# Optimization experiments

Hardware: AMD Instinct MI355X
Metric: run time of the kernel (lower is better)

Reference implementation:

```python
import jax, jax.numpy as jnp
import numpy as np

H, DQS, DQP, DVS, DVP = 12, 16, 4, 16, 8
S_SCALAR = (3.0 * DQS) ** -0.5
S_POINT = (3.0 * DQP * (9.0 * 2.0 ** 0.5)) ** -0.5
S_PAIR = 3.0 ** -0.5
_OFF = np.cumsum([0, H * DQS, H * DQS, H * DVS, H * DQP * 3, H * DQP * 3, H * DVP * 3])


def _ln(x, g, b, eps=1e-5):
    mu = x.mean(-1, keepdims=True)
    var = x.var(-1, keepdims=True)
    return (x - mu) / jnp.sqrt(var + eps) * g + b


def setup_inputs() -> dict:
    B, N, D, PD = 2, 512, 384, 128
    key = jax.random.key(0)
    ks = jax.random.split(key, 12)
    node_feats = jax.random.normal(ks[0], (B, N, D), jnp.float32)
    pair_feats = jax.random.normal(ks[1], (B, N, N, PD), jnp.float32)
    mask = jnp.ones((B, N), dtype=bool)
    # random per-residue rigid frames (orthonormal rotations via QR)
    rot = jnp.linalg.qr(jax.random.normal(ks[2], (B, N, 3, 3), jnp.float32))[0]
    trans = jax.random.normal(ks[3], (B, N, 3), jnp.float32)
    dim_qkv = int(_OFF[-1])             # 1152
    dim_out = H * (PD + DVS + 4 * DVP)  # 2112
    s = 0.02
    p = dict(
        ln_s_g=jnp.ones((D,)), ln_s_b=jnp.zeros((D,)),
        ln_p_g=jnp.ones((PD,)), ln_p_b=jnp.zeros((PD,)),
        w_pair_bias=s * jax.random.normal(ks[4], (PD, H), jnp.float32),
        w_qkv=s * jax.random.normal(ks[5], (D, dim_qkv), jnp.float32),
        point_weights=jnp.full((1, H, 1, 1), float(np.log(np.e - 1.0)), jnp.float32),
        w_out=s * jax.random.normal(ks[6], (dim_out, D), jnp.float32),
        b_out=jnp.zeros((D,)),
        ln_t_g=jnp.ones((D,)), ln_t_b=jnp.zeros((D,)),
        w_ff1=s * jax.random.normal(ks[7], (D, 4 * D), jnp.float32),
        b_ff1=jnp.zeros((4 * D,)),
        w_ff2=s * jax.random.normal(ks[8], (4 * D, D), jnp.float32),
        b_ff2=jnp.zeros((D,)),
    )
    return dict(node_feats=node_feats, pair_feats=pair_feats, mask=mask,
                rot=rot, trans=trans, **p)


def reference(node_feats, pair_feats, mask, rot, trans,
              ln_s_g, ln_s_b, ln_p_g, ln_p_b, w_pair_bias, w_qkv,
              point_weights, w_out, b_out,
              ln_t_g, ln_t_b, w_ff1, b_ff1, w_ff2, b_ff2):
    b, n, d = node_feats.shape
    x = _ln(node_feats, ln_s_g, ln_s_b)
    p = _ln(pair_feats, ln_p_g, ln_p_b)
    pair_bias = jnp.einsum('bijd,dh->bhij', p, w_pair_bias)
    qkv = x @ w_qkv  # (b,n,1152)

    def heads(t, dh):
        return t.reshape(b, n, H, dh).transpose(0, 2, 1, 3)  # b h n d

    q_s = heads(qkv[..., _OFF[0]:_OFF[1]], DQS)
    k_s = heads(qkv[..., _OFF[1]:_OFF[2]], DQS)
    v_s = heads(qkv[..., _OFF[2]:_OFF[3]], DVS)

    def to_pts(t, dp):
        pts = t.reshape(b, n, H * dp, 3)
        # rigid apply: R_i @ x + t_i (global frame)
        pts = jnp.einsum('bnxy,bnpy->bnpx', rot, pts) + trans[:, :, None, :]
        return pts.reshape(b, n, H, dp, 3).transpose(0, 2, 1, 3, 4)  # b h n d 3

    q_p = to_pts(qkv[..., _OFF[3]:_OFF[4]], DQP)
    k_p = to_pts(qkv[..., _OFF[4]:_OFF[5]], DQP)
    v_p = to_pts(qkv[..., _OFF[5]:_OFF[6]], DVP)

    scalar_logits = jnp.einsum('bhid,bhjd->bhij', q_s, k_s)
    # dist attn: -sum_{d,c} (q-k)^2, expanded to avoid (b,h,n,n,d,3) intermediate
    qq = jnp.sum(q_p * q_p, axis=(-1, -2))
    kk = jnp.sum(k_p * k_p, axis=(-1, -2))
    qk = jnp.einsum('bhidc,bhjdc->bhij', q_p, k_p)
    point_logits = -(qq[..., :, None] + kk[..., None, :] - 2.0 * qk)
    point_logits = point_logits * jax.nn.softplus(point_weights)

    neg = jnp.finfo(node_feats.dtype).min
    pm = mask[:, None, :, None] & mask[:, None, None, :]  # b 1 i j
    scalar_logits = jnp.where(pm, scalar_logits, neg)
    point_logits = jnp.where(pm, point_logits, neg)
    pair_bias = jnp.where(pm, pair_bias, neg)

    logits = S_SCALAR * scalar_logits + S_POINT * point_logits + S_PAIR * pair_bias
    attn = jax.nn.softmax(logits, axis=-1)

    out_s = jnp.einsum('bhij,bhjd->bhid', attn, v_s)
    out_pair = jnp.einsum('bhij,bijd->bhid', attn, p)
    out_p = jnp.einsum('bhij,bhjdc->bhidc', attn, v_p)
    # rigid inverse: R_i^T (x - t_i) back to local frame
    pts = out_p.transpose(0, 2, 1, 3, 4).reshape(b, n, H * DVP, 3)
    pts = jnp.einsum('bnyx,bnpy->bnpx', rot, pts - trans[:, :, None, :])
    out_p = pts.reshape(b, n, H, DVP, 3)
    pnorm = jnp.sqrt(jnp.sum(out_p * out_p, axis=-1) + 1e-8)  # safe_norm

    cat = jnp.concatenate([
        out_s.transpose(0, 2, 1, 3).reshape(b, n, H * DVS),
        out_p.reshape(b, n, H * DVP * 3),
        pnorm.reshape(b, n, H * DVP),
        out_pair.transpose(0, 2, 1, 3).reshape(b, n, -1),
    ], axis=-1)
    attn_out = cat @ w_out + b_out

    # residuals + transition (dropout=0 -> identity). Note: transition is
    # applied to attn_out (pre-residual), exactly as in the torch forward.
    node1 = attn_out + node_feats
    t = _ln(attn_out, ln_t_g, ln_t_b)
    t = jax.nn.gelu(t @ w_ff1 + b_ff1) @ w_ff2 + b_ff2
    return t + node1
```

## Files before the change

### kernel.cpp

```cpp
#include <hip/hip_runtime.h>
#include <hip/hip_bf16.h>
#include <math.h>

typedef __hip_bfloat16 bf16;
typedef _Float16 f16;
typedef unsigned short ushort_t;
typedef ushort_t ushort8 __attribute__((ext_vector_type(8)));
typedef ushort_t us4 __attribute__((ext_vector_type(4)));
typedef short bf16x8 __attribute__((ext_vector_type(8)));
typedef f16 f16x8 __attribute__((ext_vector_type(8)));
typedef f16 f16x2 __attribute__((ext_vector_type(2)));
typedef float f32x4 __attribute__((ext_vector_type(4)));
typedef unsigned int u32x4 __attribute__((ext_vector_type(4)));

constexpr float S_SCALAR = 0.14433756729740643f;
constexpr float S_POINT  = 0.08091531528f;
constexpr float S_PAIR   = 0.5773502691896258f;

__device__ inline short f2bfs(float x) {
  return (short)__builtin_bit_cast(unsigned short, __float2bfloat16(x));
}
__device__ inline ushort_t f2bfu(float x) {
  return (ushort_t)__builtin_bit_cast(unsigned short, __float2bfloat16(x));
}
__device__ inline ushort_t f2hu(float x) {
  return __builtin_bit_cast(ushort_t, (f16)x);
}
__device__ inline float h2f(ushort_t u) {
  return (float)__builtin_bit_cast(f16, u);
}
__device__ inline float fdot2f(unsigned a, unsigned b, float c) {
#if __has_builtin(__builtin_amdgcn_fdot2)
  return __builtin_amdgcn_fdot2(__builtin_bit_cast(f16x2, a),
                                __builtin_bit_cast(f16x2, b), c, false);
#else
  f16x2 av = __builtin_bit_cast(f16x2, a), bv = __builtin_bit_cast(f16x2, b);
  return c + (float)av[0] * (float)bv[0] + (float)av[1] * (float)bv[1];
#endif
}

__device__ inline float gelu_tanh(float x) {
  float c = 0.7978845608028654f * (x + 0.044715f * x * x * x);
  return 0.5f * x * (1.f + tanhf(c));
}

__global__ __launch_bounds__(128) void ln384_kernel(
    const float* __restrict__ in, const float* __restrict__ g,
    const float* __restrict__ b, float* __restrict__ out)
{
  int row = blockIdx.x;
  const float* x = in + (size_t)row * 384;
  int t = threadIdx.x;
  float v[3]; float s = 0.f, s2 = 0.f;
#pragma unroll
  for (int i = 0; i < 3; i++) { v[i] = x[t + 128 * i]; s += v[i]; s2 += v[i] * v[i]; }
  for (int o = 32; o; o >>= 1) { s += __shfl_down(s, o); s2 += __shfl_down(s2, o); }
  __shared__ float sh[4];
  int wid = t >> 6, lane = t & 63;
  if (lane == 0) { sh[wid] = s; sh[2 + wid] = s2; }
  __syncthreads();
  s = sh[0] + sh[1]; s2 = sh[2] + sh[3];
  float mean = s * (1.f / 384.f);
  float var = s2 * (1.f / 384.f) - mean * mean;
  float rstd = rsqrtf(fmaxf(var, 0.f) + 1e-5f);
  float* orow = out + (size_t)row * 384;
#pragma unroll
  for (int i = 0; i < 3; i++) {
    int c = t + 128 * i;
    orow[c] = (v[i] - mean) * rstd * g[c] + b[c];
  }
}

__global__ __launch_bounds__(256) void prep_all_kernel(
    const float* __restrict__ w_qkv, const float* __restrict__ w_out,
    const float* __restrict__ w_ff1, const float* __restrict__ w_ff2,
    ushort_t* __restrict__ wqkvT, ushort_t* __restrict__ woutT,
    ushort_t* __restrict__ wff1T, ushort_t* __restrict__ wff2T,
    const float* __restrict__ g, const float* __restrict__ bb,
    const float* __restrict__ wpb, ushort_t* __restrict__ gwbT,
    float* __restrict__ gsbs,
    const float* __restrict__ node, const float* __restrict__ ln_s_g,
    const float* __restrict__ ln_s_b, float* __restrict__ xout)
{
  __shared__ float shmem[2048];
  int bid = blockIdx.x;
  int t = threadIdx.x;
  if (bid < 2376) {
    const float* src; ushort_t* dst; int K, N, bx, by;
    if (bid < 432)       { src = w_qkv; dst = wqkvT; K = 384;  N = 1152; bx = bid % 36;          by = bid / 36; }
    else if (bid < 1224) { src = w_out; dst = woutT; K = 2112; N = 384;  bx = (bid - 432) % 12;  by = (bid - 432) / 12; }
    else if (bid < 1800) { src = w_ff1; dst = wff1T; K = 384;  N = 1536; bx = (bid - 1224) % 48; by = (bid - 1224) / 48; }
    else                 { src = w_ff2; dst = wff2T; K = 1536; N = 384;  bx = (bid - 1800) % 12; by = (bid - 1800) / 12; }
    float (&tile)[32][33] = *reinterpret_cast<float (*)[32][33]>(shmem);
    int n0 = bx * 32, k0 = by * 32;
    int c = t & 31, r4 = (t >> 5) * 4;
#pragma unroll
    for (int i = 0; i < 4; i++)
      tile[r4 + i][c] = src[(size_t)(k0 + r4 + i) * N + n0 + c];
    __syncthreads();
#pragma unroll
    for (int i = 0; i < 4; i++)
      dst[(size_t)(n0 + r4 + i) * K + k0 + c] = f2bfu(tile[c][r4 + i]);
    return;
  }
  if (bid == 2376) {
    for (int idx = t; idx < 2048; idx += 256) {
      int h = idx >> 7, c = idx & 127;
      float v = (h < 12) ? g[c] * wpb[c * 12 + h] : 0.f;
      bf16 r = __float2bfloat16(v);
      gwbT[idx] = __builtin_bit_cast(unsigned short, r);
      shmem[idx] = __bfloat162float(r);
    }
    __syncthreads();
    if (t < 16) {
      float s = 0.f;
      for (int c = 0; c < 128; c++) s += shmem[t * 128 + c];
      gsbs[t] = s;
    } else if (t < 32) {
      int h = t - 16;
      float s = 0.f;
      if (h < 12) for (int c = 0; c < 128; c++) s = fmaf(bb[c], wpb[c * 12 + h], s);
      gsbs[t] = s;
    }
    return;
  }
  int half = t >> 7, tt = t & 127;
  int row = (bid - 2377) * 2 + half;
  const float* x = node + (size_t)row * 384;
  float v[3]; float s = 0.f, s2 = 0.f;
#pragma unroll
  for (int i = 0; i < 3; i++) { v[i] = x[tt + 128 * i]; s += v[i]; s2 += v[i] * v[i]; }
  for (int o = 32; o; o >>= 1) { s += __shfl_down(s, o); s2 += __shfl_down(s2, o); }
  int wid = t >> 6, lane = t & 63;
  if (lane == 0) { shmem[wid] = s; shmem[4 + wid] = s2; }
  __syncthreads();
  s = shmem[half * 2] + shmem[half * 2 + 1];
  s2 = shmem[4 + half * 2] + shmem[4 + half * 2 + 1];
  float mean = s * (1.f / 384.f);
  float var = s2 * (1.f / 384.f) - mean * mean;
  float rstd = rsqrtf(fmaxf(var, 0.f) + 1e-5f);
  float* orow = xout + (size_t)row * 384;
#pragma unroll
  for (int i = 0; i < 3; i++) {
    int c = tt + 128 * i;
    orow[c] = (v[i] - mean) * rstd * ln_s_g[c] + ln_s_b[c];
  }
}

template <int EPI>
__global__ __launch_bounds__(256) void gemm_mfma_kernel(
    const float* __restrict__ A, const ushort_t* __restrict__ BT,
    const float* __restrict__ bias, const float* __restrict__ r1,
    const float* __restrict__ r2, float* __restrict__ C,
    int M, int Nn, int K)
{
  __shared__ ushort_t As[64][72];
  __shared__ ushort_t Bs[64][72];
  int t = threadIdx.x;
  int w = t >> 6, l = t & 63;
  int m0 = blockIdx.y * 64, n0 = blockIdx.x * 64;
  int wm = (w >> 1) * 32, wn = (w & 1) * 32;
  int lr = l & 15, lk = l >> 4;
  int sr = t >> 2, sc = (t & 3) * 16;
  f32x4 acc[2][2];
#pragma unroll
  for (int i = 0; i < 2; i++)
#pragma unroll
    for (int j = 0; j < 2; j++) acc[i][j] = (f32x4){0.f, 0.f, 0.f, 0.f};

  for (int k0 = 0; k0 < K; k0 += 64) {
    const float* Ar = A + (size_t)(m0 + sr) * K + k0 + sc;
    const ushort_t* Br = BT + (size_t)(n0 + sr) * K + k0 + sc;
    float4 a0 = *(const float4*)(Ar + 0);
    float4 a1 = *(const float4*)(Ar + 4);
    float4 a2 = *(const float4*)(Ar + 8);
    float4 a3 = *(const float4*)(Ar + 12);
    ushort8 b0 = *(const ushort8*)(Br + 0);
    ushort8 b1 = *(const ushort8*)(Br + 8);
    ushort8 u0, u1;
    u0[0] = f2bfu(a0.x); u0[1] = f2bfu(a0.y); u0[2] = f2bfu(a0.z); u0[3] = f2bfu(a0.w);
    u0[4] = f2bfu(a1.x); u0[5] = f2bfu(a1.y); u0[6] = f2bfu(a1.z); u0[7] = f2bfu(a1.w);
    u1[0] = f2bfu(a2.x); u1[1] = f2bfu(a2.y); u1[2] = f2bfu(a2.z); u1[3] = f2bfu(a2.w);
    u1[4] = f2bfu(a3.x); u1[5] = f2bfu(a3.y); u1[6] = f2bfu(a3.z); u1[7] = f2bfu(a3.w);
    *(ushort8*)&As[sr][sc] = u0;
    *(ushort8*)&As[sr][sc + 8] = u1;
    *(ushort8*)&Bs[sr][sc] = b0;
    *(ushort8*)&Bs[sr][sc + 8] = b1;
    __syncthreads();
#pragma unroll
    for (int kk = 0; kk < 2; kk++) {
      bf16x8 af0 = *(const bf16x8*)&As[wm + lr][kk * 32 + lk * 8];
      bf16x8 af1 = *(const bf16x8*)&As[wm + 16 + lr][kk * 32 + lk * 8];
      bf16x8 bf0 = *(const bf16x8*)&Bs[wn + lr][kk * 32 + lk * 8];
      bf16x8 bf1 = *(const bf16x8*)&Bs[wn + 16 + lr][kk * 32 + lk * 8];
      acc[0][0] = __builtin_amdgcn_mfma_f32_16x16x32_bf16(af0, bf0, acc[0][0], 0, 0, 0);
      acc[0][1] = __builtin_amdgcn_mfma_f32_16x16x32_bf16(af0, bf1, acc[0][1], 0, 0, 0);
      acc[1][0] = __builtin_amdgcn_mfma_f32_16x16x32_bf16(af1, bf0, acc[1][0], 0, 0, 0);
      acc[1][1] = __builtin_amdgcn_mfma_f32_16x16x32_bf16(af1, bf1, acc[1][1], 0, 0, 0);
    }
    __syncthreads();
  }
#pragma unroll
  for (int mf = 0; mf < 2; mf++) {
#pragma unroll
    for (int nf = 0; nf < 2; nf++) {
      int nn = n0 + wn + nf * 16 + lr;
      float bv = bias ? bias[nn] : 0.f;
#pragma unroll
      for (int e = 0; e < 4; e++) {
        int m = m0 + wm + mf * 16 + lk * 4 + e;
        float v = acc[mf][nf][e] + bv;
        if (EPI == 1) v = gelu_tanh(v);
        if (EPI == 2) v += r1[(size_t)m * Nn + nn] + r2[(size_t)m * Nn + nn];
        C[(size_t)m * Nn + nn] = v;
      }
    }
  }
}

template <int EPI>
__global__ __launch_bounds__(256) void gemm_mfma_m32_kernel(
    const float* __restrict__ A, const ushort_t* __restrict__ BT,
    const float* __restrict__ bias, const float* __restrict__ r1,
    const float* __restrict__ r2, float* __restrict__ C,
    int M, int Nn, int K)
{
  __shared__ ushort_t As[32][72];
  __shared__ ushort_t Bs[64][72];
  int t = threadIdx.x;
  int w = t >> 6, l = t & 63;
  int m0 = blockIdx.y * 32, n0 = blockIdx.x * 64;
  int wm = (w & 1) * 16, wn = (w >> 1) * 32;
  int lr = l & 15, lk = l >> 4;
  int ar = t >> 3, ac = (t & 7) * 8;
  int br = t >> 2, bc = (t & 3) * 16;
  f32x4 acc[2];
  acc[0] = (f32x4){0.f, 0.f, 0.f, 0.f};
  acc[1] = (f32x4){0.f, 0.f, 0.f, 0.f};

  for (int k0 = 0; k0 < K; k0 += 64) {
    const float* Ar = A + (size_t)(m0 + ar) * K + k0 + ac;
    float4 a0 = *(const float4*)(Ar + 0);
    float4 a1 = *(const float4*)(Ar + 4);
    ushort8 u;
    u[0] = f2bfu(a0.x); u[1] = f2bfu(a0.y); u[2] = f2bfu(a0.z); u[3] = f2bfu(a0.w);
    u[4] = f2bfu(a1.x); u[5] = f2bfu(a1.y); u[6] = f2bfu(a1.z); u[7] = f2bfu(a1.w);
    *(ushort8*)&As[ar][ac] = u;
    const ushort_t* Br = BT + (size_t)(n0 + br) * K + k0 + bc;
    *(ushort8*)&Bs[br][bc] = *(const ushort8*)(Br + 0);
    *(ushort8*)&Bs[br][bc + 8] = *(const ushort8*)(Br + 8);
    __syncthreads();
#pragma unroll
    for (int kk = 0; kk < 2; kk++) {
      bf16x8 af = *(const bf16x8*)&As[wm + lr][kk * 32 + lk * 8];
      bf16x8 bf0 = *(const bf16x8*)&Bs[wn + lr][kk * 32 + lk * 8];
      bf16x8 bf1 = *(const bf16x8*)&Bs[wn + 16 + lr][kk * 32 + lk * 8];
      acc[0] = __builtin_amdgcn_mfma_f32_16x16x32_bf16(af, bf0, acc[0], 0, 0, 0);
      acc[1] = __builtin_amdgcn_mfma_f32_16x16x32_bf16(af, bf1, acc[1], 0, 0, 0);
    }
    __syncthreads();
  }
#pragma unroll
  for (int nf = 0; nf < 2; nf++) {
    int nn = n0 + wn + nf * 16 + lr;
    float bv = bias ? bias[nn] : 0.f;
#pragma unroll
    for (int e = 0; e < 4; e++) {
      int m = m0 + wm + lk * 4 + e;
      float v = acc[nf][e] + bv;
      if (EPI == 1) v = gelu_tanh(v);
      if (EPI == 2) v += r1[(size_t)m * Nn + nn] + r2[(size_t)m * Nn + nn];
      C[(size_t)m * Nn + nn] = v;
    }
  }
}

__global__ __launch_bounds__(256) void qkv_post_kernel(
    const float* __restrict__ qkv, const float* __restrict__ rot,
    const float* __restrict__ trans, const float* __restrict__ pw,
    f16* __restrict__ qhat, ushort_t* __restrict__ khatP,
    ushort_t* __restrict__ vT)
{
  int bh = blockIdx.x;
  int b = bh / 12, h = bh - b * 12;
  int role = blockIdx.y >> 1;
  int j = (blockIdx.y & 1) * 256 + threadIdx.x;
  int bn = b * 512 + j;
  const float* row = qkv + (size_t)bn * 1152;
  float R[9];
#pragma unroll
  for (int k = 0; k < 9; k++) R[k] = rot[bn * 9 + k];
  float T0 = trans[bn * 3], T1 = trans[bn * 3 + 1], T2 = trans[bn * 3 + 2];
  if (role == 0) {
    float sp = log1pf(__expf(pw[h]));
    float c1 = 2.f * S_POINT * sp;
    float spp = S_POINT * sp;
    f16* qh = qhat + ((size_t)bh * 512 + j) * 32;
#pragma unroll
    for (int d = 0; d < 16; d++) qh[d] = (f16)(S_SCALAR * row[h * 16 + d]);
#pragma unroll
    for (int p = 0; p < 4; p++) {
      int base = 576 + (h * 4 + p) * 3;
      float x = row[base], y = row[base + 1], z = row[base + 2];
      qh[16 + p * 3 + 0] = (f16)(c1 * (R[0] * x + R[1] * y + R[2] * z + T0));
      qh[16 + p * 3 + 1] = (f16)(c1 * (R[3] * x + R[4] * y + R[5] * z + T1));
      qh[16 + p * 3 + 2] = (f16)(c1 * (R[6] * x + R[7] * y + R[8] * z + T2));
    }
    qh[28] = (f16)(-spp);
    qh[29] = (f16)0.f; qh[30] = (f16)0.f; qh[31] = (f16)0.f;
  } else if (role == 1) {
    float kv[32];
#pragma unroll
    for (int d = 0; d < 16; d++) kv[d] = row[192 + h * 16 + d];
    float kksum = 0.f;
#pragma unroll
    for (int p = 0; p < 4; p++) {
      int base = 720 + (h * 4 + p) * 3;
      float x = row[base], y = row[base + 1], z = row[base + 2];
      float gx = R[0] * x + R[1] * y + R[2] * z + T0;
      float gy = R[3] * x + R[4] * y + R[5] * z + T1;
      float gz = R[6] * x + R[7] * y + R[8] * z + T2;
      kv[16 + p * 3 + 0] = gx; kv[16 + p * 3 + 1] = gy; kv[16 + p * 3 + 2] = gz;
      kksum = fmaf(gx, gx, kksum); kksum = fmaf(gy, gy, kksum); kksum = fmaf(gz, gz, kksum);
    }
    kv[28] = kksum; kv[29] = 0.f; kv[30] = 0.f; kv[31] = 0.f;
    ushort_t* kp = khatP + ((size_t)bh * 4) * 512 * 8 + (size_t)j * 8;
#pragma unroll
    for (int dg = 0; dg < 4; dg++) {
      ushort8 u;
#pragma unroll
      for (int e = 0; e < 8; e++) u[e] = f2hu(kv[dg * 8 + e]);
      *(ushort8*)(kp + (size_t)dg * 512 * 8) = u;
    }
  } else {
    ushort_t* vt = vT + (size_t)bh * 40 * 512;
#pragma unroll
    for (int c = 0; c < 16; c++) vt[c * 512 + j] = f2hu(row[384 + h * 16 + c]);
#pragma unroll
    for (int p = 0; p < 8; p++) {
      int base = 864 + (h * 8 + p) * 3;
      float x = row[base], y = row[base + 1], z = row[base + 2];
      vt[(16 + p * 3 + 0) * 512 + j] = f2hu(R[0] * x + R[1] * y + R[2] * z + T0);
      vt[(16 + p * 3 + 1) * 512 + j] = f2hu(R[3] * x + R[4] * y + R[5] * z + T1);
      vt[(16 + p * 3 + 2) * 512 + j] = f2hu(R[6] * x + R[7] * y + R[8] * z + T2);
    }
  }
}

__global__ __launch_bounds__(256, 2) void mega_kernel(
    const float* __restrict__ pair, const ushort_t* __restrict__ gwbT,
    const float* __restrict__ gsbs, const float* __restrict__ g,
    const float* __restrict__ bb, const f16* __restrict__ qhat,
    const ushort_t* __restrict__ khatP, ushort_t* __restrict__ attnb,
    float* __restrict__ cat)
{
  __shared__ ushort_t tile[128][136];
  __shared__ ushort_t Ps[12][520];
  __shared__ ushort_t bias_s[12][136];
  __shared__ unsigned qhat_u[12][16];
  __shared__ float m_s[12], l_s[12], r_s[16], invl_s[12];
  __shared__ float mhist_s[4][12], cf_s[4][12];

  int bn = blockIdx.x;
  int b = bn >> 9, i = bn & 511;
  int t = threadIdx.x;
  int wv = t >> 6, ln = t & 63, lr = ln & 15, lk = ln >> 4;

  if (t < 12) { m_s[t] = -3.0e38f; l_s[t] = 0.f; }
  if (t < 16) r_s[t] = 1.f;
  if (t < 192) {
    int h = t >> 4, d4 = t & 15;
    qhat_u[h][d4] = ((const unsigned*)qhat)[((size_t)(b * 12 + h) * 512 + i) * 16 + d4];
  }
  float gsum = gsbs[lr];
  float bsP = S_PAIR * gsbs[16 + lr];
  int n0 = wv * 32;
  int sw0 = (((n0 + lr) >> 3) & 7) << 4;
  int sw1 = (((n0 + 16 + lr) >> 3) & 7) << 4;
  f32x4 po0 = {0.f, 0.f, 0.f, 0.f}, po1 = {0.f, 0.f, 0.f, 0.f};

  const float* pbase = pair + ((size_t)bn * 512 + wv * 32 + lr) * 128 + lk * 8;
  const ushort_t* gwrow = gwbT + lr * 128 + lk * 8;
  __syncthreads();

  for (int ck = 0; ck < 4; ck++) {
    int jc = ck * 128;
    const float* p0 = pbase + (size_t)ck * 16384;
    f32x4 acc0 = {0.f, 0.f, 0.f, 0.f}, acc1 = {0.f, 0.f, 0.f, 0.f};
    float s0 = 0.f, s20 = 0.f, s1 = 0.f, s21 = 0.f;
#pragma unroll
    for (int kc = 0; kc < 4; kc++) {
      us4 q0 = *(const us4*)(gwrow + kc * 32);
      us4 q1 = *(const us4*)(gwrow + kc * 32 + 4);
      bf16x8 bfr;
      bfr[0] = (short)q0[0]; bfr[1] = (short)q0[1];
      bfr[2] = (short)q0[2]; bfr[3] = (short)q0[3];
      bfr[4] = (short)q1[0]; bfr[5] = (short)q1[1];
      bfr[6] = (short)q1[2]; bfr[7] = (short)q1[3];
      float4 u0 = *(const float4*)(p0 + kc * 32);
      float4 u1 = *(const float4*)(p0 + kc * 32 + 4);
      float4 w0 = *(const float4*)(p0 + 2048 + kc * 32);
      float4 w1 = *(const float4*)(p0 + 2048 + kc * 32 + 4);
      s0 += u0.x + u0.y + u0.z + u0.w + u1.x + u1.y + u1.z + u1.w;
      s20 = fmaf(u0.x, u0.x, s20); s20 = fmaf(u0.y, u0.y, s20);
      s20 = fmaf(u0.z, u0.z, s20); s20 = fmaf(u0.w, u0.w, s20);
      s20 = fmaf(u1.x, u1.x, s20); s20 = fmaf(u1.y, u1.y, s20);
      s20 = fmaf(u1.z, u1.z, s20); s20 = fmaf(u1.w, u1.w, s20);
      s1 += w0.x + w0.y + w0.z + w0.w + w1.x + w1.y + w1.z + w1.w;
      s21 = fmaf(w0.x, w0.x, s21); s21 = fmaf(w0.y, w0.y, s21);
      s21 = fmaf(w0.z, w0.z, s21); s21 = fmaf(w0.w, w0.w, s21);
      s21 = fmaf(w1.x, w1.x, s21); s21 = fmaf(w1.y, w1.y, s21);
      s21 = fmaf(w1.z, w1.z, s21); s21 = fmaf(w1.w, w1.w, s21);
      bf16x8 a0, a1;
      a0[0] = f2bfs(u0.x); a0[1] = f2bfs(u0.y); a0[2] = f2bfs(u0.z); a0[3] = f2bfs(u0.w);
      a0[4] = f2bfs(u1.x); a0[5] = f2bfs(u1.y); a0[6] = f2bfs(u1.z); a0[7] = f2bfs(u1.w);
      a1[0] = f2bfs(w0.x); a1[1] = f2bfs(w0.y); a1[2] = f2bfs(w0.z); a1[3] = f2bfs(w0.w);
      a1[4] = f2bfs(w1.x); a1[5] = f2bfs(w1.y); a1[6] = f2bfs(w1.z); a1[7] = f2bfs(w1.w);
      acc0 = __builtin_amdgcn_mfma_f32_16x16x32_bf16(a0, bfr, acc0, 0, 0, 0);
      acc1 = __builtin_amdgcn_mfma_f32_16x16x32_bf16(a1, bfr, acc1, 0, 0, 0);
    }
    s0 += __shfl_xor(s0, 16);  s0 += __shfl_xor(s0, 32);
    s20 += __shfl_xor(s20, 16); s20 += __shfl_xor(s20, 32);
    s1 += __shfl_xor(s1, 16);  s1 += __shfl_xor(s1, 32);
    s21 += __shfl_xor(s21, 16); s21 += __shfl_xor(s21, 32);
    float mean0 = s0 * (1.f / 128.f);
    float rstd0 = rsqrtf(fmaxf(s20 * (1.f / 128.f) - mean0 * mean0, 0.f) + 1e-5f);
    float mean1 = s1 * (1.f / 128.f);
    float rstd1 = rsqrtf(fmaxf(s21 * (1.f / 128.f) - mean1 * mean1, 0.f) + 1e-5f);
    int jl_u = wv * 32 + lr, jl_w = wv * 32 + 16 + lr;
#pragma unroll
    for (int kc = 0; kc < 4; kc++) {
      int c0 = kc * 32 + lk * 8;
      float4 u0 = *(const float4*)(p0 + kc * 32);
      float4 u1 = *(const float4*)(p0 + kc * 32 + 4);
      float4 w0 = *(const float4*)(p0 + 2048 + kc * 32);
      float4 w1 = *(const float4*)(p0 + 2048 + kc * 32 + 4);
      float4 g0 = *(const float4*)(g + c0);
      float4 g1 = *(const float4*)(g + c0 + 4);
      float4 b0 = *(const float4*)(bb + c0);
      float4 b1 = *(const float4*)(bb + c0 + 4);
      float uu[8] = {u0.x, u0.y, u0.z, u0.w, u1.x, u1.y, u1.z, u1.w};
      float ww[8] = {w0.x, w0.y, w0.z, w0.w, w1.x, w1.y, w1.z, w1.w};
      float gg[8] = {g0.x, g0.y, g0.z, g0.w, g1.x, g1.y, g1.z, g1.w};
      float bv[8] = {b0.x, b0.y, b0.z, b0.w, b1.x, b1.y, b1.z, b1.w};
#pragma unroll
      for (int e = 0; e < 8; e++) {
        int c = c0 + e;
        int sw = ((c >> 3) & 7) << 4;
        tile[c][jl_u ^ sw] = f2hu(fmaf((uu[e] - mean0) * rstd0, gg[e], bv[e]));
        tile[c][jl_w ^ sw] = f2hu(fmaf((ww[e] - mean1) * rstd1, gg[e], bv[e]));
      }
    }
    {
      us4 pk0, pk1;
#pragma unroll
      for (int e = 0; e < 4; e++) {
        int r = lk * 4 + e;
        float m0 = __shfl(mean0, r), rs0 = __shfl(rstd0, r);
        float m1 = __shfl(mean1, r), rs1 = __shfl(rstd1, r);
        pk0[e] = f2hu(fmaf(S_PAIR * rs0, acc0[e] - m0 * gsum, bsP));
        pk1[e] = f2hu(fmaf(S_PAIR * rs1, acc1[e] - m1 * gsum, bsP));
      }
      if (lr < 12) {
        *(us4*)&bias_s[lr][wv * 32 + lk * 4] = pk0;
        *(us4*)&bias_s[lr][wv * 32 + 16 + lk * 4] = pk1;
      }
    }
    __syncthreads();
#pragma unroll
    for (int q = 0; q < 3; q++) {
      int h = wv + q * 4;
      const u32x4* kp = (const u32x4*)khatP + (size_t)(b * 12 + h) * 4 * 512;
      float d0 = 0.f, d1 = 0.f;
#pragma unroll
      for (int dg = 0; dg < 4; dg++) {
        u32x4 qv = *(const u32x4*)&qhat_u[h][dg * 4];
        u32x4 k0 = kp[dg * 512 + jc + ln];
        u32x4 k1 = kp[dg * 512 + jc + 64 + ln];
        d0 = fdot2f(k0[0], qv[0], d0); d0 = fdot2f(k0[1], qv[1], d0);
        d0 = fdot2f(k0[2], qv[2], d0); d0 = fdot2f(k0[3], qv[3], d0);
        d1 = fdot2f(k1[0], qv[0], d1); d1 = fdot2f(k1[1], qv[1], d1);
        d1 = fdot2f(k1[2], qv[2], d1); d1 = fdot2f(k1[3], qv[3], d1);
      }
      d0 += h2f(bias_s[h][ln]);
      d1 += h2f(bias_s[h][64 + ln]);
      float lm = fmaxf(d0, d1);
      lm = fmaxf(lm, __shfl_xor(lm, 1));  lm = fmaxf(lm, __shfl_xor(lm, 2));
      lm = fmaxf(lm, __shfl_xor(lm, 4));  lm = fmaxf(lm, __shfl_xor(lm, 8));
      lm = fmaxf(lm, __shfl_xor(lm, 16)); lm = fmaxf(lm, __shfl_xor(lm, 32));
      float mo = m_s[h];
      float mn = fmaxf(mo, lm);
      float r = __expf(mo - mn);
      float p0v = __expf(d0 - mn), p1v = __expf(d1 - mn);
      Ps[h][jc + ln] = f2hu(p0v);
      Ps[h][jc + 64 + ln] = f2hu(p1v);
      float s = p0v + p1v;
      s += __shfl_xor(s, 1);  s += __shfl_xor(s, 2);
      s += __shfl_xor(s, 4);  s += __shfl_xor(s, 8);
      s += __shfl_xor(s, 16); s += __shfl_xor(s, 32);
      if (ln == 0) {
        m_s[h] = mn; l_s[h] = l_s[h] * r + s; r_s[h] = r; mhist_s[ck][h] = mn;
      }
    }
    __syncthreads();
#pragma unroll
    for (int e = 0; e < 4; e++) {
      float rr = r_s[lk * 4 + e];
      po0[e] *= rr; po1[e] *= rr;
    }
    int arow_c = (lr < 12) ? lr : 11;
#pragma unroll
    for (int ks = 0; ks < 4; ks++) {
      int kb = ks * 32 + lk * 8;
      f16x8 af = *(const f16x8*)&Ps[arow_c][jc + kb];
      f16x8 b0 = *(const f16x8*)&tile[n0 + lr][kb ^ sw0];
      f16x8 b1 = *(const f16x8*)&tile[n0 + 16 + lr][kb ^ sw1];
      po0 = __builtin_amdgcn_mfma_f32_16x16x32_f16(af, b0, po0, 0, 0, 0);
      po1 = __builtin_amdgcn_mfma_f32_16x16x32_f16(af, b1, po1, 0, 0, 0);
    }
    __syncthreads();
  }
  if (t < 48) {
    int c = t / 12, h = t - c * 12;
    cf_s[c][h] = __expf(mhist_s[c][h] - m_s[h]);
  }
  if (t < 12) invl_s[t] = 1.f / l_s[t];
  __syncthreads();
  ushort_t* arow = attnb + (size_t)bn * 12 * 512;
#pragma unroll
  for (int it = 0; it < 24; it++) {
    int idx = t + 256 * it;
    int h = idx >> 9, j = idx & 511;
    float v = h2f(Ps[h][j]) * cf_s[j >> 7][h] * invl_s[h];
    arow[(size_t)h * 512 + j] = f2hu(v);
  }
  float* crow = cat + (size_t)bn * 2112 + 576;
#pragma unroll
  for (int e = 0; e < 4; e++) {
    int hh = lk * 4 + e;
    if (hh < 12) {
      float il = invl_s[hh];
      crow[hh * 128 + n0 + lr] = po0[e] * il;
      crow[hh * 128 + n0 + 16 + lr] = po1[e] * il;
    }
  }
}

__global__ __launch_bounds__(256) void sv_gemm_kernel(
    const ushort_t* __restrict__ attn, const ushort_t* __restrict__ vT,
    float* __restrict__ svraw)
{
  int i0 = blockIdx.x * 64;
  int bh = blockIdx.y;
  int b = bh / 12, h = bh - b * 12;
  __shared__ ushort_t As_[64][72];
  __shared__ ushort_t Bs_[48][72];
  int t = threadIdx.x;
  int w = t >> 6, l = t & 63, lr = l & 15, lk = l >> 4;
  int ai = t >> 2, as = (t & 3) * 16;
  const ushort_t* vbase = vT + (size_t)bh * 40 * 512;
  f32x4 acc[3];
#pragma unroll
  for (int n = 0; n < 3; n++) acc[n] = (f32x4){0.f, 0.f, 0.f, 0.f};

  for (int jt = 0; jt < 8; jt++) {
    int jb = jt * 64;
    size_t aoff = ((size_t)(b * 512 + i0 + ai) * 12 + h) * 512 + jb + as;
    ushort8 a0 = *(const ushort8*)(attn + aoff);
    ushort8 a1 = *(const ushort8*)(attn + aoff + 8);
    *(ushort8*)&As_[ai][as] = a0;
    *(ushort8*)&As_[ai][as + 8] = a1;
    for (int idx = t; idx < 384; idx += 256) {
      int c = idx >> 3, j8 = (idx & 7) * 8;
      ushort8 v = {0, 0, 0, 0, 0, 0, 0, 0};
      if (c < 40) v = *(const ushort8*)(vbase + (size_t)c * 512 + jb + j8);
      *(ushort8*)&Bs_[c][j8] = v;
    }
    __syncthreads();
#pragma unroll
    for (int kk = 0; kk < 2; kk++) {
      f16x8 af = *(const f16x8*)&As_[w * 16 + lr][kk * 32 + lk * 8];
#pragma unroll
      for (int n = 0; n < 3; n++) {
        f16x8 bf_ = *(const f16x8*)&Bs_[n * 16 + lr][kk * 32 + lk * 8];
        acc[n] = __builtin_amdgcn_mfma_f32_16x16x32_f16(af, bf_, acc[n], 0, 0, 0);
      }
    }
    __syncthreads();
  }
#pragma unroll
  for (int n = 0; n < 3; n++) {
    int c = n * 16 + lr;
    if (c < 40) {
#pragma unroll
      for (int e = 0; e < 4; e++) {
        int i = i0 + w * 16 + lk * 4 + e;
        svraw[(size_t)(b * 512 + i) * 480 + h * 40 + c] = acc[n][e];
      }
    }
  }
}

__global__ __launch_bounds__(192) void sv_epilogue_kernel(
    const float* __restrict__ svraw, const float* __restrict__ rot,
    const float* __restrict__ trans, float* __restrict__ cat)
{
  int bn = blockIdx.x;
  const float* sv = svraw + (size_t)bn * 480;
  float* crow = cat + (size_t)bn * 2112;
  int t = threadIdx.x;
  {
    int h2 = t >> 4, d = t & 15;
    crow[t] = sv[h2 * 40 + d];
  }
  if (t < 96) {
    int h2 = t >> 3, dp = t & 7;
    float T0 = trans[bn * 3], T1 = trans[bn * 3 + 1], T2 = trans[bn * 3 + 2];
    const float* R = rot + bn * 9;
    float px = sv[h2 * 40 + 16 + dp * 3 + 0] - T0;
    float py = sv[h2 * 40 + 16 + dp * 3 + 1] - T1;
    float pz = sv[h2 * 40 + 16 + dp * 3 + 2] - T2;
    float lx = R[0] * px + R[3] * py + R[6] * pz;
    float ly = R[1] * px + R[4] * py + R[7] * pz;
    float lz = R[2] * px + R[5] * py + R[8] * pz;
    crow[192 + h2 * 24 + dp * 3 + 0] = lx;
    crow[192 + h2 * 24 + dp * 3 + 1] = ly;
    crow[192 + h2 * 24 + dp * 3 + 2] = lz;
    crow[480 + h2 * 8 + dp] = sqrtf(lx * lx + ly * ly + lz * lz + 1e-8f);
  }
}

extern "C" void kernel_launch(void* const* d_in, const int* in_sizes, int n_in,
                              void* d_out, int out_size, void* d_ws, size_t ws_size,
                              hipStream_t stream)
{
  const float* node   = (const float*)d_in[0];
  const float* pair   = (const float*)d_in[1];
  const float* rot    = (const float*)d_in[3];
  const float* trans  = (const float*)d_in[4];
  const float* ln_s_g = (const float*)d_in[5];
  const float* ln_s_b = (const float*)d_in[6];
  const float* ln_p_g = (const float*)d_in[7];
  const float* ln_p_b = (const float*)d_in[8];
  const float* wpb    = (const float*)d_in[9];
  const float* w_qkv  = (const float*)d_in[10];
  const float* pw     = (const float*)d_in[11];
  const float* w_out  = (const float*)d_in[12];
  const float* b_out  = (const float*)d_in[13];
  const float* ln_t_g = (const float*)d_in[14];
  const float* ln_t_b = (const float*)d_in[15];
  const float* w_ff1  = (const float*)d_in[16];
  const float* b_ff1  = (const float*)d_in[17];
  const float* w_ff2  = (const float*)d_in[18];
  const float* b_ff2  = (const float*)d_in[19];
  float* out = (float*)d_out;
  float* ws = (float*)d_ws;

  float* qkv    = ws;
  float* x      = ws + 1179648;
  float* tn     = x;
  float* ao     = ws + 1572864;
  float* svraw  = ws + 1966080;
  float* cat    = ws + 2457600;
  ushort_t* attnb = (ushort_t*)(ws + 5603328);
  float* gb     = ws + 5603328;
  ushort_t* gwbT = (ushort_t*)(ws + 8749056);
  float* gsbs   = ws + 8750080;
  ushort_t* wqkvT = (ushort_t*)(ws + 8750112);
  ushort_t* woutT = (ushort_t*)(ws + 8971296);
  ushort_t* wff1T = (ushort_t*)(ws + 9376800);
  ushort_t* wff2T = (ushort_t*)(ws + 9671712);
  f16* qhat     = (f16*)(ws + 9966624);
  ushort_t* khatP = (ushort_t*)(ws + 10163232);
  ushort_t* vT  = (ushort_t*)(ws + 10359840);

  prep_all_kernel<<<2889, 256, 0, stream>>>(w_qkv, w_out, w_ff1, w_ff2,
      wqkvT, woutT, wff1T, wff2T, ln_p_g, ln_p_b, wpb, gwbT, gsbs,
      node, ln_s_g, ln_s_b, x);
  gemm_mfma_kernel<0><<<dim3(18, 16), 256, 0, stream>>>(x, wqkvT, nullptr, nullptr, nullptr, qkv, 1024, 1152, 384);
  qkv_post_kernel<<<dim3(24, 6), 256, 0, stream>>>(qkv, rot, trans, pw, qhat, khatP, vT);
  mega_kernel<<<1024, 256, 0, stream>>>(pair, gwbT, gsbs, ln_p_g, ln_p_b, qhat, khatP, attnb, cat);
  sv_gemm_kernel<<<dim3(8, 24), 256, 0, stream>>>(attnb, vT, svraw);
  sv_epilogue_kernel<<<1024, 192, 0, stream>>>(svraw, rot, trans, cat);
  gemm_mfma_m32_kernel<0><<<dim3(6, 32), 256, 0, stream>>>(cat, woutT, b_out, nullptr, nullptr, ao, 1024, 384, 2112);
  ln384_kernel<<<1024, 128, 0, stream>>>(ao, ln_t_g, ln_t_b, tn);
  gemm_mfma_kernel<1><<<dim3(24, 16), 256, 0, stream>>>(tn, wff1T, b_ff1, nullptr, nullptr, gb, 1024, 1536, 384);
  gemm_mfma_m32_kernel<2><<<dim3(6, 32), 256, 0, stream>>>(gb, wff2T, b_ff2, ao, node, out, 1024, 384, 1536);
}
```

Measured before the change: 557.0 us.

## Store QKV GEMM output transposed so qkv_post reads are coalesced

```diff
diff --git a/kernel.cpp b/kernel.cpp
--- a/kernel.cpp
+++ b/kernel.cpp
@@ -212,7 +212,8 @@
         float v = acc[mf][nf][e] + bv;
         if (EPI == 1) v = gelu_tanh(v);
         if (EPI == 2) v += r1[(size_t)m * Nn + nn] + r2[(size_t)m * Nn + nn];
-        C[(size_t)m * Nn + nn] = v;
+        if (EPI == 3) C[(size_t)nn * M + m] = v;
+        else          C[(size_t)m * Nn + nn] = v;
       }
     }
   }
@@ -276,7 +277,7 @@
 }
 
 __global__ __launch_bounds__(256) void qkv_post_kernel(
-    const float* __restrict__ qkv, const float* __restrict__ rot,
+    const float* __restrict__ qkvT, const float* __restrict__ rot,
     const float* __restrict__ trans, const float* __restrict__ pw,
     f16* __restrict__ qhat, ushort_t* __restrict__ khatP,
     ushort_t* __restrict__ vT)
@@ -284,24 +285,34 @@
   int bh = blockIdx.x;
   int b = bh / 12, h = bh - b * 12;
   int role = blockIdx.y >> 1;
-  int j = (blockIdx.y & 1) * 256 + threadIdx.x;
+  int jb2 = blockIdx.y & 1;
+  int t = threadIdx.x;
+  int j = jb2 * 256 + t;
   int bn = b * 512 + j;
-  const float* row = qkv + (size_t)bn * 1152;
+  int bn0 = b * 512 + jb2 * 256;
+  __shared__ float rotL[256][9];
+  __shared__ float trnL[256][3];
+  for (int idx = t; idx < 2304; idx += 256)
+    rotL[idx / 9][idx % 9] = rot[(size_t)bn0 * 9 + idx];
+  for (int idx = t; idx < 768; idx += 256)
+    trnL[idx / 3][idx % 3] = trans[(size_t)bn0 * 3 + idx];
+  __syncthreads();
   float R[9];
 #pragma unroll
-  for (int k = 0; k < 9; k++) R[k] = rot[bn * 9 + k];
-  float T0 = trans[bn * 3], T1 = trans[bn * 3 + 1], T2 = trans[bn * 3 + 2];
+  for (int k = 0; k < 9; k++) R[k] = rotL[t][k];
+  float T0 = trnL[t][0], T1 = trnL[t][1], T2 = trnL[t][2];
+#define QC(c) qkvT[(size_t)(c) * 1024 + bn]
   if (role == 0) {
     float sp = log1pf(__expf(pw[h]));
     float c1 = 2.f * S_POINT * sp;
     float spp = S_POINT * sp;
     f16* qh = qhat + ((size_t)bh * 512 + j) * 32;
 #pragma unroll
-    for (int d = 0; d < 16; d++) qh[d] = (f16)(S_SCALAR * row[h * 16 + d]);
+    for (int d = 0; d < 16; d++) qh[d] = (f16)(S_SCALAR * QC(h * 16 + d));
 #pragma unroll
     for (int p = 0; p < 4; p++) {
       int base = 576 + (h * 4 + p) * 3;
-      float x = row[base], y = row[base + 1], z = row[base + 2];
+      float x = QC(base), y = QC(base + 1), z = QC(base + 2);
       qh[16 + p * 3 + 0] = (f16)(c1 * (R[0] * x + R[1] * y + R[2] * z + T0));
       qh[16 + p * 3 + 1] = (f16)(c1 * (R[3] * x + R[4] * y + R[5] * z + T1));
       qh[16 + p * 3 + 2] = (f16)(c1 * (R[6] * x + R[7] * y + R[8] * z + T2));
@@ -311,12 +322,12 @@
   } else if (role == 1) {
     float kv[32];
 #pragma unroll
-    for (int d = 0; d < 16; d++) kv[d] = row[192 + h * 16 + d];
+    for (int d = 0; d < 16; d++) kv[d] = QC(192 + h * 16 + d);
     float kksum = 0.f;
 #pragma unroll
     for (int p = 0; p < 4; p++) {
       int base = 720 + (h * 4 + p) * 3;
-      float x = row[base], y = row[base + 1], z = row[base + 2];
+      float x = QC(base), y = QC(base + 1), z = QC(base + 2);
       float gx = R[0] * x + R[1] * y + R[2] * z + T0;
       float gy = R[3] * x + R[4] * y + R[5] * z + T1;
       float gz = R[6] * x + R[7] * y + R[8] * z + T2;
@@ -335,16 +346,17 @@
   } else {
     ushort_t* vt = vT + (size_t)bh * 40 * 512;
 #pragma unroll
-    for (int c = 0; c < 16; c++) vt[c * 512 + j] = f2hu(row[384 + h * 16 + c]);
+    for (int c = 0; c < 16; c++) vt[c * 512 + j] = f2hu(QC(384 + h * 16 + c));
 #pragma unroll
     for (int p = 0; p < 8; p++) {
       int base = 864 + (h * 8 + p) * 3;
-      float x = row[base], y = row[base + 1], z = row[base + 2];
+      float x = QC(base), y = QC(base + 1), z = QC(base + 2);
       vt[(16 + p * 3 + 0) * 512 + j] = f2hu(R[0] * x + R[1] * y + R[2] * z + T0);
       vt[(16 + p * 3 + 1) * 512 + j] = f2hu(R[3] * x + R[4] * y + R[5] * z + T1);
       vt[(16 + p * 3 + 2) * 512 + j] = f2hu(R[6] * x + R[7] * y + R[8] * z + T2);
     }
   }
+#undef QC
 }
 
 __global__ __launch_bounds__(256, 2) void mega_kernel(
@@ -656,7 +668,7 @@
   float* out = (float*)d_out;
   float* ws = (float*)d_ws;
 
-  float* qkv    = ws;
+  float* qkvT   = ws;
   float* x      = ws + 1179648;
   float* tn     = x;
   float* ao     = ws + 1572864;
@@ -677,8 +689,8 @@
   prep_all_kernel<<<2889, 256, 0, stream>>>(w_qkv, w_out, w_ff1, w_ff2,
       wqkvT, woutT, wff1T, wff2T, ln_p_g, ln_p_b, wpb, gwbT, gsbs,
       node, ln_s_g, ln_s_b, x);
-  gemm_mfma_kernel<0><<<dim3(18, 16), 256, 0, stream>>>(x, wqkvT, nullptr, nullptr, nullptr, qkv, 1024, 1152, 384);
-  qkv_post_kernel<<<dim3(24, 6), 256, 0, stream>>>(qkv, rot, trans, pw, qhat, khatP, vT);
+  gemm_mfma_kernel<3><<<dim3(18, 16), 256, 0, stream>>>(x, wqkvT, nullptr, nullptr, nullptr, qkvT, 1024, 1152, 384);
+  qkv_post_kernel<<<dim3(24, 6), 256, 0, stream>>>(qkvT, rot, trans, pw, qhat, khatP, vT);
   mega_kernel<<<1024, 256, 0, stream>>>(pair, gwbT, gsbs, ln_p_g, ln_p_b, qhat, khatP, attnb, cat);
   sv_gemm_kernel<<<dim3(8, 24), 256, 0, stream>>>(attnb, vT, svraw);
   sv_epilogue_kernel<<<1024, 192, 0, stream>>>(svraw, rot, trans, cat);
```

Result: no change. 561.0 us (+0.7%).
